# Performance work log

Measured on AMD Instinct MI355X. Metric: run time of the kernel, lower is better.

Reference implementation:

```python
import jax, jax.numpy as jnp
import numpy as np
from jax import lax

DN = ('NCHW', 'OIHW', 'NCHW')

def _conv(x, w, b):
    y = lax.conv_general_dilated(x, w, (1, 1), 'SAME', dimension_numbers=DN)
    return y + b[None, :, None, None]

def setup_inputs() -> dict:
    key = jax.random.key(0)
    ks = jax.random.split(key, 12)
    B, C, H, W = 8, 32, 128, 128
    Cb, INT, K, FK = 64, 64, 3, 3
    inp = {
        'z': jax.random.normal(ks[0], (B, C, H, W), jnp.float32),
        'backbone': jax.random.normal(ks[1], (B, Cb, H, W), jnp.float32),
        'mem_stab': jax.random.normal(ks[2], (B, C, H, W), jnp.float32),
        'mem_unstab': jax.random.normal(ks[3], (B, C, H, W), jnp.float32),
        'w0': jax.random.normal(ks[4], (INT, Cb + 3 * C, K, K), jnp.float32) * 0.05,
        'b0': jnp.zeros((INT,), jnp.float32),
        'w1': jax.random.normal(ks[5], (INT, INT, K, K), jnp.float32) * 0.05,
        'b1': jnp.zeros((INT,), jnp.float32),
        'w2': jax.random.normal(ks[6], (INT, INT, K, K), jnp.float32) * 0.05,
        'b2': jnp.zeros((INT,), jnp.float32),
        'w_last': jax.random.normal(ks[7], (C * FK * FK, INT, K, K), jnp.float32) * 0.05,
        'b_last': jnp.full((C * FK * FK,), -4.0, jnp.float32),
        'fusion_kernel_size': FK,
    }
    return inp

def reference(z, backbone, mem_stab, mem_unstab, w0, b0, w1, b1, w2, b2, w_last, b_last, fusion_kernel_size):
    B, C, H, W = z.shape
    k = int(fusion_kernel_size)
    p = k * k
    # controller conv stack (LeakyReLU slope 0.01, matching nn.LeakyReLU default)
    q = jnp.concatenate([backbone, z, mem_stab, mem_unstab], axis=1)
    q = jax.nn.leaky_relu(_conv(q, w0, b0), 0.01)
    q = jax.nn.leaky_relu(_conv(q, w1, b1), 0.01)
    q = jax.nn.leaky_relu(_conv(q, w2, b2), 0.01)
    # fusion head -> [B, C, p, HW]
    head = _conv(q, w_last, b_last).reshape(B, C, p, H * W)
    # softmax over p kernel positions + one extra logit-0 slot for z itself
    eta = jax.nn.softmax(jnp.concatenate([head, jnp.zeros_like(head[:, :, :1])], axis=2), axis=2)
    # unfold(mem_stab, k, padding=k//2): patches ordered (c, kh, kw) like torch unfold
    pad = k // 2
    mpad = jnp.pad(mem_stab, ((0, 0), (0, 0), (pad, pad), (pad, pad)))
    patches = jnp.stack([mpad[:, :, i:i + H, j:j + W] for i in range(k) for j in range(k)], axis=2)
    patches = patches.reshape(B, C, p, H * W)
    z_flat = z.reshape(B, C, H * W)
    z_stab = (patches * eta[:, :, :p]).sum(axis=2) + eta[:, :, p] * z_flat
    return z_stab.reshape(B, C, H, W)
```

## Files before the change

### kernel.cpp

```cpp
#include <hip/hip_runtime.h>
#include <hip/hip_fp16.h>

typedef _Float16 half8 __attribute__((ext_vector_type(8)));
typedef _Float16 half4v __attribute__((ext_vector_type(4)));
typedef float floatx4 __attribute__((ext_vector_type(4)));

#define HW 128
#define IMG (HW * HW)
#define PH 130
#define XP 164

typedef __attribute__((address_space(3))) _Float16 lds_f16;
typedef __attribute__((address_space(1))) const _Float16 glb_f16;
__device__ __forceinline__ void gload16(const _Float16* g, _Float16* l) {
    __builtin_amdgcn_global_load_lds((glb_f16*)g, (lds_f16*)l, 16, 0, 0);
}

__global__ void pack_w_all(const float* __restrict__ w0, const float* __restrict__ w1,
                           const float* __restrict__ w2, const float* __restrict__ wl,
                           _Float16* __restrict__ p0, _Float16* __restrict__ p1,
                           _Float16* __restrict__ p2, _Float16* __restrict__ pl) {
    int idx = blockIdx.x * 256 + threadIdx.x;
    if (idx < 92160) {
        int local = idx;
        int o = local / 1440;
        int rem = local % 1440;
        int c = rem / 9;
        int t = rem % 9;
        int oh = o >> 5, n = (o >> 4) & 1, l15 = o & 15;
        int cb = c >> 5, l4 = (c >> 3) & 3, e = c & 7;
        int frag = (t * 5 + cb) * 2 + n;
        p0[(size_t)oh * 46080 + frag * 512 + (l4 * 16 + l15) * 8 + e] =
            (_Float16)w0[local];
        return;
    }
    if (idx < 165888) {
        const float* w; _Float16* p; int local;
        if (idx < 129024) { w = w1; p = p1; local = idx - 92160; }
        else              { w = w2; p = p2; local = idx - 129024; }
        int o = local / 576;
        int rem = local % 576;
        int c = rem / 9;
        int t = rem % 9;
        int oh = o >> 5, n = (o >> 4) & 1, l15 = o & 15;
        int cb = c >> 5, l4 = (c >> 3) & 3, e = c & 7;
        int frag = t * 4 + cb * 2 + n;
        p[(size_t)oh * 18432 + frag * 512 + (l4 * 16 + l15) * 8 + e] =
            (_Float16)w[local];
        return;
    }
    if (idx < 331776) {
        int local = idx - 165888;
        int of = local / 576;
        int rem = local % 576;
        int c = rem / 9;
        int t = rem % 9;
        int g = of / 48;
        int n = (of % 48) / 16;
        int l15 = of & 15;
        int j = c >> 3;
        int cb = j >> 2, l4 = j & 3, e = c & 7;
        int frag = t * 2 + cb;
        pl[((((size_t)g * 18 + frag) * 3 + n) * 64
            + (l4 * 16 + l15)) * 8 + e] = (_Float16)wl[local];
    }
}

__global__ __launch_bounds__(256)
void pack_in(const float* __restrict__ z, const float* __restrict__ bb,
             const float* __restrict__ ms, const float* __restrict__ mu,
             _Float16* __restrict__ X0) {
    __shared__ _Float16 lds[160 * 132];
    int b = blockIdx.x >> 7;
    int h = blockIdx.x & 127;
    int tid = threadIdx.x;

    for (int i = 0; i < 20; i++) {
        int id = i * 256 + tid;
        int c = id >> 5;
        int col = (id & 31) * 4;
        const float* src; int cs; int csz;
        if (c < 64)       { src = bb; cs = c;       csz = 64; }
        else if (c < 96)  { src = z;  cs = c - 64;  csz = 32; }
        else if (c < 128) { src = ms; cs = c - 96;  csz = 32; }
        else              { src = mu; cs = c - 128; csz = 32; }
        float4 v = *reinterpret_cast<const float4*>(
            src + ((size_t)b * csz + cs) * IMG + h * HW + col);
        half4v hv = { (_Float16)v.x, (_Float16)v.y, (_Float16)v.z, (_Float16)v.w };
        *reinterpret_cast<half4v*>(&lds[c * 132 + col]) = hv;
    }
    __syncthreads();
    _Float16* dst = X0 + (((size_t)b * PH + (h + 1)) * PH + 1) * 160;
    for (int i = 0; i < 10; i++) {
        int id = i * 256 + tid;
        int pix = id / 20;
        int c0 = (id % 20) * 8;
        half8 hv;
        #pragma unroll
        for (int e = 0; e < 8; e++) hv[e] = lds[(c0 + e) * 132 + pix];
        *reinterpret_cast<half8*>(dst + (size_t)pix * 160 + c0) = hv;
    }

    half8 z8 = {};
    _Float16* rowp = X0 + (((size_t)b * PH + (h + 1)) * PH) * 160;
    if (tid < 40) {
        int col = (tid < 20) ? 0 : 129;
        int v = (tid < 20) ? tid : tid - 20;
        *reinterpret_cast<half8*>(rowp + (size_t)col * 160 + v * 8) = z8;
    }
    if (h == 0 || h == 127) {
        int prow = (h == 0) ? 0 : 129;
        _Float16* rp = X0 + (((size_t)b * PH + prow) * PH) * 160;
        for (int i = tid; i < 2600; i += 256)
            *reinterpret_cast<half8*>(rp + (size_t)i * 8) = z8;
    }
}

__global__ __launch_bounds__(256, 2)
void conv3_c160(const _Float16* __restrict__ X, const _Float16* __restrict__ Wp,
                const float* __restrict__ bias, _Float16* __restrict__ Y) {
    __shared__ _Float16 xs[130 * XP];
    int b = blockIdx.x >> 7;
    int h = blockIdx.x & 127;
    int tid = threadIdx.x;
    int lane = tid & 63;
    int wave = tid >> 6;
    int ph = wave & 1;
    int oh = wave >> 1;
    int l15 = lane & 15;
    int l4  = lane >> 4;

    floatx4 acc[4][2] = {};
    half8 SA[10], SB[10];

    const _Float16* wl = Wp + (size_t)oh * 46080 + lane * 8;

#define LOADW(S, k) { \
    _Pragma("unroll") \
    for (int cb = 0; cb < 5; cb++) \
      _Pragma("unroll") \
      for (int n = 0; n < 2; n++) \
        S[cb * 2 + n] = *reinterpret_cast<const half8*>( \
            wl + (size_t)(((k) * 5 + cb) * 2 + n) * 512); }

#define STAGE160(r) { \
    const _Float16* grow = X + ((size_t)b * PH + (h + (r))) * PH * 160; \
    _Pragma("unroll") \
    for (int i = 0; i < 11; i++) { \
      int id = i * 256 + tid; \
      if (id < 2600) { \
        half8 v = *reinterpret_cast<const half8*>(grow + (size_t)id * 8); \
        *reinterpret_cast<half8*>(&xs[(id / 20) * XP + (id % 20) * 8]) = v; \
      } } }

#define COMP160(dw, S) { \
    _Pragma("unroll") \
    for (int cb = 0; cb < 5; cb++) { \
      int kofs = cb * 32 + l4 * 8; \
      half8 af[4]; \
      _Pragma("unroll") \
      for (int m = 0; m < 4; m++) { \
        int p = ph * 64 + m * 16 + l15; \
        af[m] = *reinterpret_cast<const half8*>(&xs[(p + (dw)) * XP + kofs]); \
      } \
      _Pragma("unroll") \
      for (int m = 0; m < 4; m++) \
        _Pragma("unroll") \
        for (int n = 0; n < 2; n++) \
          acc[m][n] = __builtin_amdgcn_mfma_f32_16x16x32_f16( \
              af[m], S[cb * 2 + n], acc[m][n], 0, 0, 0); } }

    LOADW(SA, 0);
    STAGE160(0);
    __syncthreads();
    LOADW(SB, 1);  COMP160(0, SA);
    LOADW(SA, 2);  COMP160(1, SB);
    LOADW(SB, 3);  COMP160(2, SA);
    __syncthreads();
    STAGE160(1);
    __syncthreads();
    LOADW(SA, 4);  COMP160(0, SB);
    LOADW(SB, 5);  COMP160(1, SA);
    LOADW(SA, 6);  COMP160(2, SB);
    __syncthreads();
    STAGE160(2);
    __syncthreads();
    LOADW(SB, 7);  COMP160(0, SA);
    LOADW(SA, 8);  COMP160(1, SB);
    COMP160(2, SA);

#undef LOADW
#undef STAGE160
#undef COMP160

    _Float16* dst = Y + (((size_t)b * PH + (h + 1)) * PH + 1) * 64;
    #pragma unroll
    for (int m = 0; m < 4; m++)
        #pragma unroll
        for (int n = 0; n < 2; n++) {
            int o = oh * 32 + n * 16 + l15;
            float bv = bias[o];
            #pragma unroll
            for (int q = 0; q < 4; q++) {
                int pix = ph * 64 + m * 16 + l4 * 4 + q;
                float v = acc[m][n][q] + bv;
                v = v > 0.f ? v : 0.01f * v;
                dst[(size_t)pix * 64 + o] = (_Float16)v;
            }
        }

    half8 z8 = {};
    _Float16* rowq = Y + (((size_t)b * PH + (h + 1)) * PH) * 64;
    if (tid < 16) {
        int col = (tid < 8) ? 0 : 129;
        int v = tid & 7;
        *reinterpret_cast<half8*>(rowq + (size_t)col * 64 + v * 8) = z8;
    }
    if (h == 0 || h == 127) {
        int prow = (h == 0) ? 0 : 129;
        _Float16* rp = Y + (((size_t)b * PH + prow) * PH) * 64;
        for (int i = tid; i < 1040; i += 256)
            *reinterpret_cast<half8*>(rp + (size_t)i * 8) = z8;
    }
}

__global__ __launch_bounds__(256, 2)
void conv3_c64(const _Float16* __restrict__ X, const _Float16* __restrict__ Wp,
               const float* __restrict__ bias, _Float16* __restrict__ Y) {
    __shared__ _Float16 xs[130 * 72];
    int b = blockIdx.x >> 7;
    int h = blockIdx.x & 127;
    int tid = threadIdx.x;
    int lane = tid & 63;
    int wave = tid >> 6;
    int ph = wave & 1;
    int oh = wave >> 1;
    int l15 = lane & 15;
    int l4  = lane >> 4;

    floatx4 acc[4][2] = {};
    half8 SA[4], SB[4];

    const _Float16* wl = Wp + (size_t)oh * 18432 + lane * 8;
    const _Float16* xbase = X + ((size_t)b * PH + h) * (PH * 64);

#define LOADW1(S, k) { \
    _Pragma("unroll") \
    for (int cb = 0; cb < 2; cb++) \
      _Pragma("unroll") \
      for (int n = 0; n < 2; n++) \
        S[cb * 2 + n] = *reinterpret_cast<const half8*>( \
            wl + (size_t)((k) * 4 + cb * 2 + n) * 512); }

#define STAGE64(r) { \
    const _Float16* grow = xbase + (size_t)(r) * (PH * 64); \
    _Pragma("unroll") \
    for (int i = 0; i < 5; i++) { \
      int id = i * 256 + tid; \
      if (id < 1040) { \
        half8 v = *reinterpret_cast<const half8*>(grow + (size_t)id * 8); \
        *reinterpret_cast<half8*>(&xs[(id >> 3) * 72 + (id & 7) * 8]) = v; \
      } } }

#define COMP64(dw, S) { \
    _Pragma("unroll") \
    for (int cb = 0; cb < 2; cb++) { \
      int kofs = cb * 32 + l4 * 8; \
      half8 af[4]; \
      _Pragma("unroll") \
      for (int m = 0; m < 4; m++) { \
        int p = ph * 64 + m * 16 + l15; \
        af[m] = *reinterpret_cast<const half8*>(&xs[(p + (dw)) * 72 + kofs]); \
      } \
      _Pragma("unroll") \
      for (int m = 0; m < 4; m++) \
        _Pragma("unroll") \
        for (int n = 0; n < 2; n++) \
          acc[m][n] = __builtin_amdgcn_mfma_f32_16x16x32_f16( \
              af[m], S[cb * 2 + n], acc[m][n], 0, 0, 0); } }

    LOADW1(SA, 0);
    STAGE64(0);
    __syncthreads();
    LOADW1(SB, 1);  COMP64(0, SA);
    LOADW1(SA, 2);  COMP64(1, SB);
    LOADW1(SB, 3);  COMP64(2, SA);
    __syncthreads();
    STAGE64(1);
    __syncthreads();
    LOADW1(SA, 4);  COMP64(0, SB);
    LOADW1(SB, 5);  COMP64(1, SA);
    LOADW1(SA, 6);  COMP64(2, SB);
    __syncthreads();
    STAGE64(2);
    __syncthreads();
    LOADW1(SB, 7);  COMP64(0, SA);
    LOADW1(SA, 8);  COMP64(1, SB);
    COMP64(2, SA);

#undef LOADW1
#undef STAGE64
#undef COMP64

    _Float16* dst = Y + (((size_t)b * PH + (h + 1)) * PH + 1) * 64;
    #pragma unroll
    for (int m = 0; m < 4; m++)
        #pragma unroll
        for (int n = 0; n < 2; n++) {
            int o = oh * 32 + n * 16 + l15;
            float bv = bias[o];
            #pragma unroll
            for (int q = 0; q < 4; q++) {
                int pix = ph * 64 + m * 16 + l4 * 4 + q;
                float v = acc[m][n][q] + bv;
                v = v > 0.f ? v : 0.01f * v;
                dst[(size_t)pix * 64 + o] = (_Float16)v;
            }
        }

    half8 z8 = {};
    _Float16* rowq = Y + (((size_t)b * PH + (h + 1)) * PH) * 64;
    if (tid < 16) {
        int col = (tid < 8) ? 0 : 129;
        int v = tid & 7;
        *reinterpret_cast<half8*>(rowq + (size_t)col * 64 + v * 8) = z8;
    }
    if (h == 0 || h == 127) {
        int prow = (h == 0) ? 0 : 129;
        _Float16* rp = Y + (((size_t)b * PH + prow) * PH) * 64;
        for (int i = tid; i < 1040; i += 256)
            *reinterpret_cast<half8*>(rp + (size_t)i * 8) = z8;
    }
}

__global__ __launch_bounds__(256, 2)
void head_fused(const _Float16* __restrict__ X, const _Float16* __restrict__ Wp,
                const float* __restrict__ b_last, const float* __restrict__ ms,
                const float* __restrict__ zin, float* __restrict__ out,
                _Float16* __restrict__ Ls) {
    __shared__ _Float16 smem[12672];
    _Float16* xs = smem;
    _Float16* tb = smem;
    int blk = blockIdx.x;
    int ct = blk >> 10;
    int b  = (blk >> 7) & 7;
    int h  = blk & 127;
    int tid = threadIdx.x;
    int lane = tid & 63;
    int wave = tid >> 6;
    int pxh = wave & 1;
    int og  = wave >> 1;
    int l15 = lane & 15;
    int l4  = lane >> 4;

    floatx4 acc[4][3] = {};
    half8 SA[3], SB[3];

    const _Float16* wlh = Wp + ((size_t)ct * 2 + og) * 27648 + lane * 8;
    const _Float16* xbase = X + ((size_t)b * PH + h) * (PH * 64);

#define LOADWH(S, k, cb) { \
    _Pragma("unroll") \
    for (int n = 0; n < 3; n++) \
      S[n] = *reinterpret_cast<const half8*>( \
          wlh + (size_t)(((k) * 2 + (cb)) * 3 + n) * 512); }

#define STAGEH(r) { \
    const _Float16* xrow = xbase + (size_t)(r) * (PH * 64); \
    _Pragma("unroll") \
    for (int i = 0; i < 5; i++) { \
      int sbase = i * 256 + wave * 64; \
      int s = sbase + lane; \
      if (s < 1040) { \
        int px = s >> 3; \
        int j = (s & 7) ^ (px & 7); \
        gload16(xrow + (size_t)(px * 8 + j) * 8, xs + (size_t)sbase * 8); \
      } } }

#define COMPH(dw, cb, S) { \
    int j = (cb) * 4 + l4; \
    half8 af[4]; \
    _Pragma("unroll") \
    for (int m = 0; m < 4; m++) { \
      int px = pxh * 64 + m * 16 + l15 + (dw); \
      af[m] = *reinterpret_cast<const half8*>( \
          &xs[px * 64 + (j ^ (px & 7)) * 8]); \
    } \
    _Pragma("unroll") \
    for (int m = 0; m < 4; m++) \
      _Pragma("unroll") \
      for (int n = 0; n < 3; n++) \
        acc[m][n] = __builtin_amdgcn_mfma_f32_16x16x32_f16( \
            af[m], S[n], acc[m][n], 0, 0, 0); }

    LOADWH(SA, 0, 0);
    STAGEH(0);
    __syncthreads();
    LOADWH(SB, 0, 1);  COMPH(0, 0, SA);
    LOADWH(SA, 1, 0);  COMPH(0, 1, SB);
    LOADWH(SB, 1, 1);  COMPH(1, 0, SA);
    LOADWH(SA, 2, 0);  COMPH(1, 1, SB);
    LOADWH(SB, 2, 1);  COMPH(2, 0, SA);
    LOADWH(SA, 3, 0);  COMPH(2, 1, SB);
    __syncthreads();
    STAGEH(1);
    __syncthreads();
    LOADWH(SB, 3, 1);  COMPH(0, 0, SA);
    LOADWH(SA, 4, 0);  COMPH(0, 1, SB);
    LOADWH(SB, 4, 1);  COMPH(1, 0, SA);
    LOADWH(SA, 5, 0);  COMPH(1, 1, SB);
    LOADWH(SB, 5, 1);  COMPH(2, 0, SA);
    LOADWH(SA, 6, 0);  COMPH(2, 1, SB);
    __syncthreads();
    STAGEH(2);
    __syncthreads();
    LOADWH(SB, 6, 1);  COMPH(0, 0, SA);
    LOADWH(SA, 7, 0);  COMPH(0, 1, SB);
    LOADWH(SB, 7, 1);  COMPH(1, 0, SA);
    LOADWH(SA, 8, 0);  COMPH(1, 1, SB);
    LOADWH(SB, 8, 1);  COMPH(2, 0, SA);
    COMPH(2, 1, SB);

#undef LOADWH
#undef STAGEH
#undef COMPH

    __syncthreads();

    #pragma unroll
    for (int m = 0; m < 4; m++)
        #pragma unroll
        for (int n = 0; n < 3; n++) {
            int od = og * 48 + n * 16 + l15;
            float bv = b_last[ct * 96 + od];
            half4v hv;
            #pragma unroll
            for (int q = 0; q < 4; q++) hv[q] = (_Float16)(acc[m][n][q] + bv);
            *reinterpret_cast<half4v*>(&tb[od * 132 + pxh * 64 + m * 16 + l4 * 4]) = hv;
        }
    __syncthreads();

    if (tid < 96) {
        int rowi = tid >> 4;
        int sl = tid & 15;
        int localrow, slot;
        if (ct == 0)      { localrow = 90 + rowi; slot = rowi; }
        else if (ct == 1) { localrow = (rowi < 3) ? rowi : 90 + rowi;
                            slot = 6 + rowi; }
        else              { localrow = rowi; slot = 12 + rowi; }
        half8 v = *reinterpret_cast<const half8*>(&tb[localrow * 132 + sl * 8]);
        *reinterpret_cast<half8*>(
            Ls + (((size_t)(b * 128 + h) * 18 + slot) * 128 + sl * 8)) = v;
    }

    #pragma unroll
    for (int i = 0; i < 5; i++) {
        int idx = i * 256 + tid;
        int cidx = idx >> 7;
        int px = idx & 127;
        int c = (ct == 0) ? cidx : ((ct == 1) ? 11 + cidx : 22 + cidx);
        int lbase = c * 9 - ct * 96;
        float L[9];
        float mx = 0.f;
        #pragma unroll
        for (int j = 0; j < 9; j++) {
            L[j] = (float)tb[(lbase + j) * 132 + px];
            mx = fmaxf(mx, L[j]);
        }
        float ez = __expf(-mx);
        float sum = ez;
        float e[9];
        #pragma unroll
        for (int j = 0; j < 9; j++) { e[j] = __expf(L[j] - mx); sum += e[j]; }
        float inv = 1.f / sum;
        const float* msb = ms + ((size_t)b * 32 + c) * IMG;
        float accv = ez * inv * zin[((size_t)b * 32 + c) * IMG + h * HW + px];
        #pragma unroll
        for (int kh = 0; kh < 3; kh++) {
            int h2 = h + kh - 1;
            int h2c = min(max(h2, 0), 127);
            bool okh = (unsigned)h2 < 128u;
            #pragma unroll
            for (int kw = 0; kw < 3; kw++) {
                int w2 = px + kw - 1;
                int w2c = min(max(w2, 0), 127);
                bool okw = (unsigned)w2 < 128u;
                float mv = msb[h2c * HW + w2c];
                accv += e[kh * 3 + kw] * inv * ((okh && okw) ? mv : 0.f);
            }
        }
        out[((size_t)b * 32 + c) * IMG + h * HW + px] = accv;
    }
}

__global__ __launch_bounds__(256)
void fuse_strad(const _Float16* __restrict__ Ls, const float* __restrict__ ms,
                const float* __restrict__ zin, float* __restrict__ out) {
    int blk = blockIdx.x;
    int b = blk >> 7;
    int h = blk & 127;
    int tid = threadIdx.x;
    int cs = tid >> 7;
    int px = tid & 127;
    int c = cs ? 21 : 10;
    int sb = cs ? 9 : 0;

    const _Float16* lrow = Ls + (((size_t)(b * 128 + h) * 18 + sb) * 128) + px;
    float L[9];
    float mx = 0.f;
    #pragma unroll
    for (int j = 0; j < 9; j++) { L[j] = (float)lrow[j * 128]; mx = fmaxf(mx, L[j]); }
    float ez = __expf(-mx);
    float sum = ez;
    float e[9];
    #pragma unroll
    for (int j = 0; j < 9; j++) { e[j] = __expf(L[j] - mx); sum += e[j]; }
    float inv = 1.f / sum;
    const float* msb = ms + ((size_t)b * 32 + c) * IMG;
    float accv = ez * inv * zin[((size_t)b * 32 + c) * IMG + h * HW + px];
    #pragma unroll
    for (int kh = 0; kh < 3; kh++) {
        int h2 = h + kh - 1;
        int h2c = min(max(h2, 0), 127);
        bool okh = (unsigned)h2 < 128u;
        #pragma unroll
        for (int kw = 0; kw < 3; kw++) {
            int w2 = px + kw - 1;
            int w2c = min(max(w2, 0), 127);
            bool okw = (unsigned)w2 < 128u;
            float mv = msb[h2c * HW + w2c];
            accv += e[kh * 3 + kw] * inv * ((okh && okw) ? mv : 0.f);
        }
    }
    out[((size_t)b * 32 + c) * IMG + h * HW + px] = accv;
}

extern "C" void kernel_launch(void* const* d_in, const int* in_sizes, int n_in,
                              void* d_out, int out_size, void* d_ws, size_t ws_size,
                              hipStream_t stream) {
    const float* z  = (const float*)d_in[0];
    const float* bb = (const float*)d_in[1];
    const float* ms = (const float*)d_in[2];
    const float* mu = (const float*)d_in[3];
    const float* w0 = (const float*)d_in[4];
    const float* b0 = (const float*)d_in[5];
    const float* w1 = (const float*)d_in[6];
    const float* b1 = (const float*)d_in[7];
    const float* w2 = (const float*)d_in[8];
    const float* b2 = (const float*)d_in[9];
    const float* wl = (const float*)d_in[10];
    const float* bl = (const float*)d_in[11];

    char* ws = (char*)d_ws;
    _Float16* Wp0 = (_Float16*)(ws + 0);
    _Float16* Wp1 = (_Float16*)(ws + 184320);
    _Float16* Wp2 = (_Float16*)(ws + 258048);
    _Float16* WpL = (_Float16*)(ws + 331776);
    _Float16* BufA = (_Float16*)(ws + 663552);
    _Float16* BufB = (_Float16*)(ws + 43927552);

    _Float16* X0 = BufA;
    _Float16* Q1 = BufB;
    _Float16* Q2 = BufA;
    _Float16* Q3 = BufB;
    _Float16* Ls = BufA;

    pack_w_all<<<(331776 + 255) / 256, 256, 0, stream>>>(w0, w1, w2, wl, Wp0, Wp1, Wp2, WpL);
    pack_in<<<1024, 256, 0, stream>>>(z, bb, ms, mu, X0);

    conv3_c160<<<1024, 256, 0, stream>>>(X0, Wp0, b0, Q1);
    conv3_c64<<<1024, 256, 0, stream>>>(Q1, Wp1, b1, Q2);
    conv3_c64<<<1024, 256, 0, stream>>>(Q2, Wp2, b2, Q3);

    head_fused<<<3072, 256, 0, stream>>>(Q3, WpL, bl, ms, z, (float*)d_out, Ls);
    fuse_strad<<<1024, 256, 0, stream>>>(Ls, ms, z, (float*)d_out);
}
```

Measured before the change: 158.1 us.

## Fuse input packing into first conv by staging fp32 inputs directly

```diff
diff --git a/kernel.cpp b/kernel.cpp
--- a/kernel.cpp
+++ b/kernel.cpp
@@ -66,59 +66,11 @@
     }
 }
 
-__global__ __launch_bounds__(256)
-void pack_in(const float* __restrict__ z, const float* __restrict__ bb,
-             const float* __restrict__ ms, const float* __restrict__ mu,
-             _Float16* __restrict__ X0) {
-    __shared__ _Float16 lds[160 * 132];
-    int b = blockIdx.x >> 7;
-    int h = blockIdx.x & 127;
-    int tid = threadIdx.x;
-
-    for (int i = 0; i < 20; i++) {
-        int id = i * 256 + tid;
-        int c = id >> 5;
-        int col = (id & 31) * 4;
-        const float* src; int cs; int csz;
-        if (c < 64)       { src = bb; cs = c;       csz = 64; }
-        else if (c < 96)  { src = z;  cs = c - 64;  csz = 32; }
-        else if (c < 128) { src = ms; cs = c - 96;  csz = 32; }
-        else              { src = mu; cs = c - 128; csz = 32; }
-        float4 v = *reinterpret_cast<const float4*>(
-            src + ((size_t)b * csz + cs) * IMG + h * HW + col);
-        half4v hv = { (_Float16)v.x, (_Float16)v.y, (_Float16)v.z, (_Float16)v.w };
-        *reinterpret_cast<half4v*>(&lds[c * 132 + col]) = hv;
-    }
-    __syncthreads();
-    _Float16* dst = X0 + (((size_t)b * PH + (h + 1)) * PH + 1) * 160;
-    for (int i = 0; i < 10; i++) {
-        int id = i * 256 + tid;
-        int pix = id / 20;
-        int c0 = (id % 20) * 8;
-        half8 hv;
-        #pragma unroll
-        for (int e = 0; e < 8; e++) hv[e] = lds[(c0 + e) * 132 + pix];
-        *reinterpret_cast<half8*>(dst + (size_t)pix * 160 + c0) = hv;
-    }
-
-    half8 z8 = {};
-    _Float16* rowp = X0 + (((size_t)b * PH + (h + 1)) * PH) * 160;
-    if (tid < 40) {
-        int col = (tid < 20) ? 0 : 129;
-        int v = (tid < 20) ? tid : tid - 20;
-        *reinterpret_cast<half8*>(rowp + (size_t)col * 160 + v * 8) = z8;
-    }
-    if (h == 0 || h == 127) {
-        int prow = (h == 0) ? 0 : 129;
-        _Float16* rp = X0 + (((size_t)b * PH + prow) * PH) * 160;
-        for (int i = tid; i < 2600; i += 256)
-            *reinterpret_cast<half8*>(rp + (size_t)i * 8) = z8;
-    }
-}
-
 __global__ __launch_bounds__(256, 2)
-void conv3_c160(const _Float16* __restrict__ X, const _Float16* __restrict__ Wp,
-                const float* __restrict__ bias, _Float16* __restrict__ Y) {
+void conv3_c160(const float* __restrict__ z, const float* __restrict__ bb,
+                const float* __restrict__ ms, const float* __restrict__ mu,
+                const _Float16* __restrict__ Wp, const float* __restrict__ bias,
+                _Float16* __restrict__ Y) {
     __shared__ _Float16 xs[130 * XP];
     int b = blockIdx.x >> 7;
     int h = blockIdx.x & 127;
@@ -143,15 +95,35 @@
         S[cb * 2 + n] = *reinterpret_cast<const half8*>( \
             wl + (size_t)(((k) * 5 + cb) * 2 + n) * 512); }
 
-#define STAGE160(r) { \
-    const _Float16* grow = X + ((size_t)b * PH + (h + (r))) * PH * 160; \
-    _Pragma("unroll") \
-    for (int i = 0; i < 11; i++) { \
+#define STAGE160F(r) { \
+    int ur = h + (r) - 1; \
+    bool valid = (unsigned)ur < 128u; \
+    for (int i = 0; i < 20; i++) { \
       int id = i * 256 + tid; \
-      if (id < 2600) { \
-        half8 v = *reinterpret_cast<const half8*>(grow + (size_t)id * 8); \
-        *reinterpret_cast<half8*>(&xs[(id / 20) * XP + (id % 20) * 8]) = v; \
-      } } }
+      int c = id >> 5; \
+      int q = id & 31; \
+      float4 v = make_float4(0.f, 0.f, 0.f, 0.f); \
+      if (valid) { \
+        const float* src; int cs; int csz; \
+        if (c < 64)       { src = bb; cs = c;       csz = 64; } \
+        else if (c < 96)  { src = z;  cs = c - 64;  csz = 32; } \
+        else if (c < 128) { src = ms; cs = c - 96;  csz = 32; } \
+        else              { src = mu; cs = c - 128; csz = 32; } \
+        v = *reinterpret_cast<const float4*>( \
+            src + ((size_t)b * csz + cs) * IMG + ur * HW + q * 4); \
+      } \
+      int pxb = q * 4 + 1; \
+      xs[(pxb + 0) * XP + c] = (_Float16)v.x; \
+      xs[(pxb + 1) * XP + c] = (_Float16)v.y; \
+      xs[(pxb + 2) * XP + c] = (_Float16)v.z; \
+      xs[(pxb + 3) * XP + c] = (_Float16)v.w; \
+    } \
+    if (tid < 40) { \
+      int col = (tid < 20) ? 0 : 129; \
+      int v8 = (tid < 20) ? tid : tid - 20; \
+      half8 z8 = {}; \
+      *reinterpret_cast<half8*>(&xs[col * XP + v8 * 8]) = z8; \
+    } }
 
 #define COMP160(dw, S) { \
     _Pragma("unroll") \
@@ -171,26 +143,26 @@
               af[m], S[cb * 2 + n], acc[m][n], 0, 0, 0); } }
 
     LOADW(SA, 0);
-    STAGE160(0);
+    STAGE160F(0);
     __syncthreads();
     LOADW(SB, 1);  COMP160(0, SA);
     LOADW(SA, 2);  COMP160(1, SB);
     LOADW(SB, 3);  COMP160(2, SA);
     __syncthreads();
-    STAGE160(1);
+    STAGE160F(1);
     __syncthreads();
     LOADW(SA, 4);  COMP160(0, SB);
     LOADW(SB, 5);  COMP160(1, SA);
     LOADW(SA, 6);  COMP160(2, SB);
     __syncthreads();
-    STAGE160(2);
+    STAGE160F(2);
     __syncthreads();
     LOADW(SB, 7);  COMP160(0, SA);
     LOADW(SA, 8);  COMP160(1, SB);
     COMP160(2, SA);
 
 #undef LOADW
-#undef STAGE160
+#undef STAGE160F
 #undef COMP160
 
     _Float16* dst = Y + (((size_t)b * PH + (h + 1)) * PH + 1) * 64;
@@ -559,16 +531,14 @@
     _Float16* BufA = (_Float16*)(ws + 663552);
     _Float16* BufB = (_Float16*)(ws + 43927552);
 
-    _Float16* X0 = BufA;
     _Float16* Q1 = BufB;
     _Float16* Q2 = BufA;
     _Float16* Q3 = BufB;
     _Float16* Ls = BufA;
 
     pack_w_all<<<(331776 + 255) / 256, 256, 0, stream>>>(w0, w1, w2, wl, Wp0, Wp1, Wp2, WpL);
-    pack_in<<<1024, 256, 0, stream>>>(z, bb, ms, mu, X0);
-
-    conv3_c160<<<1024, 256, 0, stream>>>(X0, Wp0, b0, Q1);
+
+    conv3_c160<<<1024, 256, 0, stream>>>(z, bb, ms, mu, Wp0, b0, Q1);
     conv3_c64<<<1024, 256, 0, stream>>>(Q1, Wp1, b1, Q2);
     conv3_c64<<<1024, 256, 0, stream>>>(Q2, Wp2, b2, Q3);
 
```

New measurement: 167.6 us. +6.0%, slower.
